# Optimization experiments

Measured on AMD Instinct MI355X. Metric: run time of the kernel, lower is better.

The kernel has to match this reference:

```python
import jax, jax.numpy as jnp
import numpy as np

N_NODES = 8192
N_EDGES = 262144
IN_F, HID, OUT_F = 512, 512, 256


def setup_inputs() -> dict:
    key = jax.random.key(0)
    k_x, k_e, k_w1, k_b1, k_w2, k_b2 = jax.random.split(key, 6)
    x = jax.random.normal(k_x, (N_NODES, IN_F), dtype=jnp.float32)
    edge_index = jax.random.randint(k_e, (2, N_EDGES), 0, N_NODES, dtype=jnp.int64)
    # xavier-uniform linear weights, stored as [in, out]
    def xavier(k, fan_in, fan_out):
        lim = np.sqrt(6.0 / (fan_in + fan_out)).astype(np.float32)
        return jax.random.uniform(k, (fan_in, fan_out), jnp.float32, -lim, lim)
    W1 = xavier(k_w1, IN_F, HID)
    b1 = jax.random.uniform(k_b1, (HID,), jnp.float32, -0.05, 0.05)
    W2 = xavier(k_w2, HID, OUT_F)
    b2 = jax.random.uniform(k_b2, (OUT_F,), jnp.float32, -0.05, 0.05)
    return {"x": x, "edge_index": edge_index, "W1": W1, "b1": b1, "W2": W2, "b2": b2}


def _gcn_layer(x, edge_index, W, b):
    # H' = D~^{-1/2} A~ D~^{-1/2} H W + b, with A~ = A + I
    n = x.shape[0]
    adj = jnp.zeros((n, n), dtype=x.dtype).at[edge_index[0], edge_index[1]].set(1.0)
    adj = adj + jnp.eye(n, dtype=x.dtype)
    degree = jnp.clip(adj.sum(axis=1), 1.0, None)
    d_inv_sqrt = degree ** -0.5
    adj_norm = adj * d_inv_sqrt[None, :] * d_inv_sqrt[:, None]
    return (adj_norm @ x) @ W + b


def reference(x, edge_index, W1, b1, W2, b2):
    h = jax.nn.relu(_gcn_layer(x, edge_index, W1, b1))
    # dropout p=0.0 -> identity
    out = _gcn_layer(h, edge_index, W2, b2)
    return out
```

## Files before the change

kernel.cpp:

```cpp
#include <hip/hip_runtime.h>
#include <hip/hip_bf16.h>
#include <stdint.h>

#define N_NODES 8192
#define N_EDGES 262144
#define IN_F 512
#define HID 512
#define OUT_F 256
#define CAP 128

typedef __attribute__((ext_vector_type(8))) short short8;
typedef __attribute__((ext_vector_type(4))) float f32x4;

__device__ __forceinline__ float bflo(unsigned int u) {
  union { unsigned int x; float f; } c; c.x = u << 16; return c.f;
}
__device__ __forceinline__ float bfhi(unsigned int u) {
  union { unsigned int x; float f; } c; c.x = u & 0xffff0000u; return c.f;
}
__device__ __forceinline__ float bf1(unsigned short s) {
  union { unsigned int x; float f; } c; c.x = (unsigned int)s << 16; return c.f;
}
__device__ __forceinline__ unsigned short f2bf(float f) {
  union { float f; unsigned int u; } c; c.f = f;
  unsigned int r = c.u + 0x7fffu + ((c.u >> 16) & 1u);
  return (unsigned short)(r >> 16);
}

__device__ __forceinline__ void gload_lds16(const void* g, void* l) {
  __builtin_amdgcn_global_load_lds((const __attribute__((address_space(1))) void*)g,
                                   (__attribute__((address_space(3))) void*)l, 16, 0, 0);
}

#define NB_CVT  4096
#define NB_W1   1024
#define NB_W2    512
#define NB_EDGE 1024
__global__ __launch_bounds__(256) void prep_all(
    const float* __restrict__ x, const float* __restrict__ W1, const float* __restrict__ W2,
    const int* __restrict__ ei,
    unsigned short* __restrict__ Xb, unsigned short* __restrict__ W1t,
    unsigned short* __restrict__ W2t, int* __restrict__ cnt, int* __restrict__ adj) {
  const int b = blockIdx.x, tid = threadIdx.x;
  if (b < NB_CVT) {
    int idx = b * 256 + tid;
    const float4 v = ((const float4*)x)[idx];
    uint2 o;
    o.x = (unsigned int)f2bf(v.x) | ((unsigned int)f2bf(v.y) << 16);
    o.y = (unsigned int)f2bf(v.z) | ((unsigned int)f2bf(v.w) << 16);
    ((uint2*)Xb)[idx] = o;
  } else if (b < NB_CVT + NB_W1) {
    int idx = (b - NB_CVT) * 256 + tid;
    int k = idx >> 9, n = idx & 511;
    W1t[n * IN_F + k] = f2bf(W1[idx]);
  } else if (b < NB_CVT + NB_W1 + NB_W2) {
    int idx = (b - NB_CVT - NB_W1) * 256 + tid;
    int k = idx >> 8, n = idx & 255;
    W2t[n * HID + k] = f2bf(W2[idx]);
  } else {
    int e = (b - NB_CVT - NB_W1 - NB_W2) * 256 + tid;
    int i = ei[e];
    int j = ei[N_EDGES + e];
    int p = atomicAdd(&cnt[i], 1);
    if (p < CAP) adj[i * CAP + p] = j;
  }
}

__global__ __launch_bounds__(128) void dedup_node(
    int* __restrict__ cnt, int* __restrict__ adj, float* __restrict__ dis) {
  const int i = blockIdx.x, t = threadIdx.x;
  __shared__ int js[CAP];
  __shared__ unsigned char keep[CAP];
  int n0 = cnt[i]; if (n0 > CAP) n0 = CAP;
  if (t < n0) js[t] = adj[i * CAP + t];
  __syncthreads();
  bool k = false;
  if (t < n0) {
    k = true;
    int jt = js[t];
    for (int s = 0; s < t; ++s) if (js[s] == jt) { k = false; break; }
  }
  keep[t] = k;
  __syncthreads();
  if (k) {
    int r = 0;
    for (int s = 0; s < t; ++s) r += keep[s];
    adj[i * CAP + r] = js[t];
  }
  if (t == 0) {
    int nd = 0;
    for (int s = 0; s < n0; ++s) nd += keep[s];
    cnt[i] = nd;
    dis[i] = rsqrtf((float)(nd + 1));
  }
}

template<int BM, int BN>
__global__ __launch_bounds__(256) void gemm_bt(
    const unsigned short* __restrict__ A, const unsigned short* __restrict__ Bt,
    unsigned short* __restrict__ C, int M, int N, int K) {
  constexpr int MR = BM / 32, NR = BN / 32;
  __shared__ __align__(16) unsigned short As[BM * 64];
  __shared__ __align__(16) unsigned short Bs[BN * 64];
  const int tid = threadIdx.x;
  const long row0 = (long)blockIdx.x * BM;
  const long col0 = (long)blockIdx.y * BN;
  const int lane = tid & 63;
  const int wid = tid >> 6;
  const int ln15 = lane & 15, hi = lane >> 4;
  const int wr = (wid >> 1) * (BM / 2), wc = (wid & 1) * (BN / 2);
  const int sr = tid >> 3;
  const int sk = (tid & 7) * 8;
  f32x4 acc[MR][NR] = {};

  for (int k0 = 0; k0 < K; k0 += 64) {
#pragma unroll
    for (int c = 0; c < MR; ++c)
      gload_lds16(A  + (row0 + c * 32 + sr) * (long)K + k0 + sk, &As[(c * 256 + tid) * 8]);
#pragma unroll
    for (int c = 0; c < NR; ++c)
      gload_lds16(Bt + (col0 + c * 32 + sr) * (long)K + k0 + sk, &Bs[(c * 256 + tid) * 8]);
    __syncthreads();
#pragma unroll
    for (int kk = 0; kk < 64; kk += 32) {
      short8 a[MR], b[NR];
#pragma unroll
      for (int m = 0; m < MR; ++m)
        a[m] = *(const short8*)&As[(wr + m * 16 + ln15) * 64 + kk + hi * 8];
#pragma unroll
      for (int n = 0; n < NR; ++n)
        b[n] = *(const short8*)&Bs[(wc + n * 16 + ln15) * 64 + kk + hi * 8];
#pragma unroll
      for (int m = 0; m < MR; ++m)
#pragma unroll
        for (int n = 0; n < NR; ++n)
          acc[m][n] = __builtin_amdgcn_mfma_f32_16x16x32_bf16(a[m], b[n], acc[m][n], 0, 0, 0);
    }
    __syncthreads();
  }
#pragma unroll
  for (int m = 0; m < MR; ++m)
#pragma unroll
    for (int n = 0; n < NR; ++n)
#pragma unroll
      for (int r = 0; r < 4; ++r) {
        long row = row0 + wr + m * 16 + hi * 4 + r;
        long col = col0 + wc + n * 16 + ln15;
        C[row * N + col] = f2bf(acc[m][n][r]);
      }
}

__global__ __launch_bounds__(256) void aggregate_relu(
    const unsigned short* __restrict__ T, const int* __restrict__ cnt,
    const int* __restrict__ adj, const float* __restrict__ dis,
    const float* __restrict__ bias, unsigned short* __restrict__ H) {
  const int i = blockIdx.x;
  const int c0 = blockIdx.y * 256;
  const int tid = threadIdx.x;
  const int lane = tid & 63, w = tid >> 6;
  __shared__ int js[CAP];
  __shared__ float ws[CAP];
  __shared__ float part[4][256];
  int n = cnt[i];
  if (tid < n) { int j = adj[i * CAP + tid]; js[tid] = j; ws[tid] = dis[j]; }
  __syncthreads();
  float a[4] = {};
  for (int e = w; e < n; e += 4) {
    const uint2 v = *(const uint2*)&T[(long)js[e] * 512 + c0 + lane * 4];
    float wj = ws[e];
    a[0] += wj * bflo(v.x); a[1] += wj * bfhi(v.x);
    a[2] += wj * bflo(v.y); a[3] += wj * bfhi(v.y);
  }
  *(float4*)&part[w][lane * 4] = make_float4(a[0], a[1], a[2], a[3]);
  __syncthreads();
  const float di = dis[i];
  float self = di * bf1(T[(long)i * 512 + c0 + tid]);
  float s = part[0][tid] + part[1][tid] + part[2][tid] + part[3][tid] + self;
  float h = fmaxf(di * s + bias[c0 + tid], 0.f);
  H[(long)i * 512 + c0 + tid] = f2bf(h);
}

__global__ __launch_bounds__(256) void aggregate_out(
    const unsigned short* __restrict__ T, const int* __restrict__ cnt,
    const int* __restrict__ adj, const float* __restrict__ dis,
    const float* __restrict__ bias, float* __restrict__ out) {
  const int i = blockIdx.x;
  const int tid = threadIdx.x;
  const int lane = tid & 63, w = tid >> 6;
  __shared__ int js[CAP];
  __shared__ float ws[CAP];
  __shared__ float part[4][256];
  int n = cnt[i];
  if (tid < n) { int j = adj[i * CAP + tid]; js[tid] = j; ws[tid] = dis[j]; }
  __syncthreads();
  float a[4] = {};
  for (int e = w; e < n; e += 4) {
    const uint2 v = *(const uint2*)&T[(long)js[e] * 256 + lane * 4];
    float wj = ws[e];
    a[0] += wj * bflo(v.x); a[1] += wj * bfhi(v.x);
    a[2] += wj * bflo(v.y); a[3] += wj * bfhi(v.y);
  }
  *(float4*)&part[w][lane * 4] = make_float4(a[0], a[1], a[2], a[3]);
  __syncthreads();
  const float di = dis[i];
  float self = di * bf1(T[(long)i * 256 + tid]);
  float s = part[0][tid] + part[1][tid] + part[2][tid] + part[3][tid] + self;
  out[(long)i * 256 + tid] = di * s + bias[tid];
}

extern "C" void kernel_launch(void* const* d_in, const int* in_sizes, int n_in,
                              void* d_out, int out_size, void* d_ws, size_t ws_size,
                              hipStream_t stream) {
  const float* x  = (const float*)d_in[0];
  const int*   ei = (const int*)d_in[1];
  const float* W1 = (const float*)d_in[2];
  const float* b1 = (const float*)d_in[3];
  const float* W2 = (const float*)d_in[4];
  const float* b2 = (const float*)d_in[5];
  float* out = (float*)d_out;

  char* ws = (char*)d_ws;
  int* cnt   = (int*)ws;                     ws += 32768;
  int* adj   = (int*)ws;                     ws += (size_t)N_NODES * CAP * 4;
  float* dis = (float*)ws;                   ws += 32768;
  unsigned short* Xb  = (unsigned short*)ws; ws += (size_t)N_NODES * IN_F * 2;
  unsigned short* W1t = (unsigned short*)ws; ws += (size_t)IN_F * HID * 2;
  unsigned short* W2t = (unsigned short*)ws; ws += (size_t)HID * OUT_F * 2;
  unsigned short* T1  = (unsigned short*)ws; ws += (size_t)N_NODES * HID * 2;
  unsigned short* H   = (unsigned short*)ws; ws += (size_t)N_NODES * HID * 2;
  unsigned short* T2  = (unsigned short*)ws; ws += (size_t)N_NODES * OUT_F * 2;

  hipMemsetAsync(cnt, 0, 32768, stream);

  prep_all<<<NB_CVT + NB_W1 + NB_W2 + NB_EDGE, 256, 0, stream>>>(
      x, W1, W2, ei, Xb, W1t, W2t, cnt, adj);
  dedup_node<<<N_NODES, 128, 0, stream>>>(cnt, adj, dis);

  gemm_bt<128, 64><<<dim3(N_NODES / 128, HID / 64), 256, 0, stream>>>(Xb, W1t, T1, N_NODES, HID, IN_F);
  aggregate_relu<<<dim3(N_NODES, 2), 256, 0, stream>>>(T1, cnt, adj, dis, b1, H);

  gemm_bt<64, 64><<<dim3(N_NODES / 64, OUT_F / 64), 256, 0, stream>>>(H, W2t, T2, N_NODES, OUT_F, HID);
  aggregate_out<<<N_NODES, 256, 0, stream>>>(T2, cnt, adj, dis, b2, out);
}
```

Before: 183.0 us.

## Map one wavefront per node in aggregation and tile weight transposes through LDS

The two aggregation kernels now give each 64-lane wavefront a whole node instead of splitting one node's edges across four waves. Each lane loads 8 or 4 bf16 columns with wide loads, the loop is unrolled by two edges, and the shared-memory partial reduction with its second barrier is gone. Launches drop to N/4 blocks. Separately, the weight bf16 transpose in prep_all now goes through a padded 64x64 LDS tile so both reads and writes are coalesced, replacing scattered 2-byte stores. The cost is less memory-level parallelism per node and possible load imbalance across high-degree nodes within a block.

```diff
diff --git a/kernel.cpp b/kernel.cpp
--- a/kernel.cpp
+++ b/kernel.cpp
@@ -18,9 +18,6 @@
 __device__ __forceinline__ float bfhi(unsigned int u) {
   union { unsigned int x; float f; } c; c.x = u & 0xffff0000u; return c.f;
 }
-__device__ __forceinline__ float bf1(unsigned short s) {
-  union { unsigned int x; float f; } c; c.x = (unsigned int)s << 16; return c.f;
-}
 __device__ __forceinline__ unsigned short f2bf(float f) {
   union { float f; unsigned int u; } c; c.f = f;
   unsigned int r = c.u + 0x7fffu + ((c.u >> 16) & 1u);
@@ -33,14 +30,43 @@
 }
 
 #define NB_CVT  4096
-#define NB_W1   1024
-#define NB_W2    512
+#define NB_W1T  64
+#define NB_W2T  32
 #define NB_EDGE 1024
+
+__device__ __forceinline__ void transpose_tile64(
+    const float* __restrict__ W, unsigned short* __restrict__ Wt,
+    int K, int N, int kb, int nb, int tid, float (*tile)[65]) {
+  const int k0g = kb * 64, n0g = nb * 64;
+  const int r = tid >> 4;
+  const int c4 = (tid & 15) * 4;
+#pragma unroll
+  for (int rr = 0; rr < 4; ++rr) {
+    const int k = rr * 16 + r;
+    const float4 v = *(const float4*)&W[(size_t)(k0g + k) * N + n0g + c4];
+    tile[k][c4] = v.x; tile[k][c4 + 1] = v.y; tile[k][c4 + 2] = v.z; tile[k][c4 + 3] = v.w;
+  }
+  __syncthreads();
+  const int n = tid >> 2;
+  const int kq = (tid & 3) * 16;
+  unsigned int o[8];
+#pragma unroll
+  for (int q = 0; q < 8; ++q) {
+    unsigned int lo = f2bf(tile[kq + 2 * q][n]);
+    unsigned int hi = f2bf(tile[kq + 2 * q + 1][n]);
+    o[q] = lo | (hi << 16);
+  }
+  unsigned int* dst = (unsigned int*)&Wt[(size_t)(n0g + n) * K + k0g + kq];
+  *(uint4*)dst       = make_uint4(o[0], o[1], o[2], o[3]);
+  *(uint4*)(dst + 4) = make_uint4(o[4], o[5], o[6], o[7]);
+}
+
 __global__ __launch_bounds__(256) void prep_all(
     const float* __restrict__ x, const float* __restrict__ W1, const float* __restrict__ W2,
     const int* __restrict__ ei,
     unsigned short* __restrict__ Xb, unsigned short* __restrict__ W1t,
     unsigned short* __restrict__ W2t, int* __restrict__ cnt, int* __restrict__ adj) {
+  __shared__ float tile[64][65];
   const int b = blockIdx.x, tid = threadIdx.x;
   if (b < NB_CVT) {
     int idx = b * 256 + tid;
@@ -49,16 +75,14 @@
     o.x = (unsigned int)f2bf(v.x) | ((unsigned int)f2bf(v.y) << 16);
     o.y = (unsigned int)f2bf(v.z) | ((unsigned int)f2bf(v.w) << 16);
     ((uint2*)Xb)[idx] = o;
-  } else if (b < NB_CVT + NB_W1) {
-    int idx = (b - NB_CVT) * 256 + tid;
-    int k = idx >> 9, n = idx & 511;
-    W1t[n * IN_F + k] = f2bf(W1[idx]);
-  } else if (b < NB_CVT + NB_W1 + NB_W2) {
-    int idx = (b - NB_CVT - NB_W1) * 256 + tid;
-    int k = idx >> 8, n = idx & 255;
-    W2t[n * HID + k] = f2bf(W2[idx]);
+  } else if (b < NB_CVT + NB_W1T) {
+    int t = b - NB_CVT;
+    transpose_tile64(W1, W1t, IN_F, HID, t >> 3, t & 7, tid, tile);
+  } else if (b < NB_CVT + NB_W1T + NB_W2T) {
+    int t = b - NB_CVT - NB_W1T;
+    transpose_tile64(W2, W2t, HID, OUT_F, t >> 2, t & 3, tid, tile);
   } else {
-    int e = (b - NB_CVT - NB_W1 - NB_W2) * 256 + tid;
+    int e = (b - NB_CVT - NB_W1T - NB_W2T) * 256 + tid;
     int i = ei[e];
     int j = ei[N_EDGES + e];
     int p = atomicAdd(&cnt[i], 1);
@@ -154,58 +178,110 @@
     const unsigned short* __restrict__ T, const int* __restrict__ cnt,
     const int* __restrict__ adj, const float* __restrict__ dis,
     const float* __restrict__ bias, unsigned short* __restrict__ H) {
-  const int i = blockIdx.x;
-  const int c0 = blockIdx.y * 256;
-  const int tid = threadIdx.x;
-  const int lane = tid & 63, w = tid >> 6;
-  __shared__ int js[CAP];
-  __shared__ float ws[CAP];
-  __shared__ float part[4][256];
-  int n = cnt[i];
-  if (tid < n) { int j = adj[i * CAP + tid]; js[tid] = j; ws[tid] = dis[j]; }
-  __syncthreads();
-  float a[4] = {};
-  for (int e = w; e < n; e += 4) {
-    const uint2 v = *(const uint2*)&T[(long)js[e] * 512 + c0 + lane * 4];
-    float wj = ws[e];
-    a[0] += wj * bflo(v.x); a[1] += wj * bfhi(v.x);
-    a[2] += wj * bflo(v.y); a[3] += wj * bfhi(v.y);
-  }
-  *(float4*)&part[w][lane * 4] = make_float4(a[0], a[1], a[2], a[3]);
-  __syncthreads();
+  const int w = threadIdx.x >> 6, lane = threadIdx.x & 63;
+  const int i = blockIdx.x * 4 + w;
+  __shared__ uint2 jw[4][CAP];
+  const int n = cnt[i];
+  for (int e0 = 0; e0 < n; e0 += 64)
+    if (e0 + lane < n) {
+      int j = adj[i * CAP + e0 + lane];
+      jw[w][e0 + lane] = make_uint2((unsigned int)j, __float_as_uint(dis[j]));
+    }
+  __syncthreads();
+  float a[8] = {};
   const float di = dis[i];
-  float self = di * bf1(T[(long)i * 512 + c0 + tid]);
-  float s = part[0][tid] + part[1][tid] + part[2][tid] + part[3][tid] + self;
-  float h = fmaxf(di * s + bias[c0 + tid], 0.f);
-  H[(long)i * 512 + c0 + tid] = f2bf(h);
+  int e = 0;
+  for (; e + 2 <= n; e += 2) {
+    const uint2 p0 = jw[w][e], p1 = jw[w][e + 1];
+    const uint4 v0 = *(const uint4*)&T[(size_t)p0.x * 512 + lane * 8];
+    const uint4 v1 = *(const uint4*)&T[(size_t)p1.x * 512 + lane * 8];
+    const float w0 = __uint_as_float(p0.y), w1 = __uint_as_float(p1.y);
+    a[0] += w0 * bflo(v0.x); a[1] += w0 * bfhi(v0.x);
+    a[2] += w0 * bflo(v0.y); a[3] += w0 * bfhi(v0.y);
+    a[4] += w0 * bflo(v0.z); a[5] += w0 * bfhi(v0.z);
+    a[6] += w0 * bflo(v0.w); a[7] += w0 * bfhi(v0.w);
+    a[0] += w1 * bflo(v1.x); a[1] += w1 * bfhi(v1.x);
+    a[2] += w1 * bflo(v1.y); a[3] += w1 * bfhi(v1.y);
+    a[4] += w1 * bflo(v1.z); a[5] += w1 * bfhi(v1.z);
+    a[6] += w1 * bflo(v1.w); a[7] += w1 * bfhi(v1.w);
+  }
+  if (e < n) {
+    const uint2 p0 = jw[w][e];
+    const uint4 v0 = *(const uint4*)&T[(size_t)p0.x * 512 + lane * 8];
+    const float w0 = __uint_as_float(p0.y);
+    a[0] += w0 * bflo(v0.x); a[1] += w0 * bfhi(v0.x);
+    a[2] += w0 * bflo(v0.y); a[3] += w0 * bfhi(v0.y);
+    a[4] += w0 * bflo(v0.z); a[5] += w0 * bfhi(v0.z);
+    a[6] += w0 * bflo(v0.w); a[7] += w0 * bfhi(v0.w);
+  }
+  {
+    const uint4 vs = *(const uint4*)&T[(size_t)i * 512 + lane * 8];
+    a[0] += di * bflo(vs.x); a[1] += di * bfhi(vs.x);
+    a[2] += di * bflo(vs.y); a[3] += di * bfhi(vs.y);
+    a[4] += di * bflo(vs.z); a[5] += di * bfhi(vs.z);
+    a[6] += di * bflo(vs.w); a[7] += di * bfhi(vs.w);
+  }
+  const float4 b0 = *(const float4*)&bias[lane * 8];
+  const float4 b1 = *(const float4*)&bias[lane * 8 + 4];
+  float h[8];
+  h[0] = fmaxf(di * a[0] + b0.x, 0.f); h[1] = fmaxf(di * a[1] + b0.y, 0.f);
+  h[2] = fmaxf(di * a[2] + b0.z, 0.f); h[3] = fmaxf(di * a[3] + b0.w, 0.f);
+  h[4] = fmaxf(di * a[4] + b1.x, 0.f); h[5] = fmaxf(di * a[5] + b1.y, 0.f);
+  h[6] = fmaxf(di * a[6] + b1.z, 0.f); h[7] = fmaxf(di * a[7] + b1.w, 0.f);
+  uint4 o;
+  o.x = (unsigned int)f2bf(h[0]) | ((unsigned int)f2bf(h[1]) << 16);
+  o.y = (unsigned int)f2bf(h[2]) | ((unsigned int)f2bf(h[3]) << 16);
+  o.z = (unsigned int)f2bf(h[4]) | ((unsigned int)f2bf(h[5]) << 16);
+  o.w = (unsigned int)f2bf(h[6]) | ((unsigned int)f2bf(h[7]) << 16);
+  *(uint4*)&H[(size_t)i * 512 + lane * 8] = o;
 }
 
 __global__ __launch_bounds__(256) void aggregate_out(
     const unsigned short* __restrict__ T, const int* __restrict__ cnt,
     const int* __restrict__ adj, const float* __restrict__ dis,
     const float* __restrict__ bias, float* __restrict__ out) {
-  const int i = blockIdx.x;
-  const int tid = threadIdx.x;
-  const int lane = tid & 63, w = tid >> 6;
-  __shared__ int js[CAP];
-  __shared__ float ws[CAP];
-  __shared__ float part[4][256];
-  int n = cnt[i];
-  if (tid < n) { int j = adj[i * CAP + tid]; js[tid] = j; ws[tid] = dis[j]; }
+  const int w = threadIdx.x >> 6, lane = threadIdx.x & 63;
+  const int i = blockIdx.x * 4 + w;
+  __shared__ uint2 jw[4][CAP];
+  const int n = cnt[i];
+  for (int e0 = 0; e0 < n; e0 += 64)
+    if (e0 + lane < n) {
+      int j = adj[i * CAP + e0 + lane];
+      jw[w][e0 + lane] = make_uint2((unsigned int)j, __float_as_uint(dis[j]));
+    }
   __syncthreads();
   float a[4] = {};
-  for (int e = w; e < n; e += 4) {
-    const uint2 v = *(const uint2*)&T[(long)js[e] * 256 + lane * 4];
-    float wj = ws[e];
-    a[0] += wj * bflo(v.x); a[1] += wj * bfhi(v.x);
-    a[2] += wj * bflo(v.y); a[3] += wj * bfhi(v.y);
-  }
-  *(float4*)&part[w][lane * 4] = make_float4(a[0], a[1], a[2], a[3]);
-  __syncthreads();
   const float di = dis[i];
-  float self = di * bf1(T[(long)i * 256 + tid]);
-  float s = part[0][tid] + part[1][tid] + part[2][tid] + part[3][tid] + self;
-  out[(long)i * 256 + tid] = di * s + bias[tid];
+  int e = 0;
+  for (; e + 2 <= n; e += 2) {
+    const uint2 p0 = jw[w][e], p1 = jw[w][e + 1];
+    const uint2 v0 = *(const uint2*)&T[(size_t)p0.x * 256 + lane * 4];
+    const uint2 v1 = *(const uint2*)&T[(size_t)p1.x * 256 + lane * 4];
+    const float w0 = __uint_as_float(p0.y), w1 = __uint_as_float(p1.y);
+    a[0] += w0 * bflo(v0.x); a[1] += w0 * bfhi(v0.x);
+    a[2] += w0 * bflo(v0.y); a[3] += w0 * bfhi(v0.y);
+    a[0] += w1 * bflo(v1.x); a[1] += w1 * bfhi(v1.x);
+    a[2] += w1 * bflo(v1.y); a[3] += w1 * bfhi(v1.y);
+  }
+  if (e < n) {
+    const uint2 p0 = jw[w][e];
+    const uint2 v0 = *(const uint2*)&T[(size_t)p0.x * 256 + lane * 4];
+    const float w0 = __uint_as_float(p0.y);
+    a[0] += w0 * bflo(v0.x); a[1] += w0 * bfhi(v0.x);
+    a[2] += w0 * bflo(v0.y); a[3] += w0 * bfhi(v0.y);
+  }
+  {
+    const uint2 vs = *(const uint2*)&T[(size_t)i * 256 + lane * 4];
+    a[0] += di * bflo(vs.x); a[1] += di * bfhi(vs.x);
+    a[2] += di * bflo(vs.y); a[3] += di * bfhi(vs.y);
+  }
+  const float4 bb = *(const float4*)&bias[lane * 4];
+  float4 o;
+  o.x = di * a[0] + bb.x;
+  o.y = di * a[1] + bb.y;
+  o.z = di * a[2] + bb.z;
+  o.w = di * a[3] + bb.w;
+  *(float4*)&out[(size_t)i * 256 + lane * 4] = o;
 }
 
 extern "C" void kernel_launch(void* const* d_in, const int* in_sizes, int n_in,
@@ -232,13 +308,13 @@
 
   hipMemsetAsync(cnt, 0, 32768, stream);
 
-  prep_all<<<NB_CVT + NB_W1 + NB_W2 + NB_EDGE, 256, 0, stream>>>(
+  prep_all<<<NB_CVT + NB_W1T + NB_W2T + NB_EDGE, 256, 0, stream>>>(
       x, W1, W2, ei, Xb, W1t, W2t, cnt, adj);
   dedup_node<<<N_NODES, 128, 0, stream>>>(cnt, adj, dis);
 
   gemm_bt<128, 64><<<dim3(N_NODES / 128, HID / 64), 256, 0, stream>>>(Xb, W1t, T1, N_NODES, HID, IN_F);
-  aggregate_relu<<<dim3(N_NODES, 2), 256, 0, stream>>>(T1, cnt, adj, dis, b1, H);
+  aggregate_relu<<<N_NODES / 4, 256, 0, stream>>>(T1, cnt, adj, dis, b1, H);
 
   gemm_bt<64, 64><<<dim3(N_NODES / 64, OUT_F / 64), 256, 0, stream>>>(H, W2t, T2, N_NODES, OUT_F, HID);
-  aggregate_out<<<N_NODES, 256, 0, stream>>>(T2, cnt, adj, dis, b2, out);
-}
+  aggregate_out<<<N_NODES / 4, 256, 0, stream>>>(T2, cnt, adj, dis, b2, out);
+}
```

Result: faster. 162.4 us (-11.2%).
